# Kernel optimization log

Hardware: AMD Instinct MI355X
Metric: run time of the kernel (lower is better)

Reference implementation:

```python
import jax, jax.numpy as jnp
import numpy as np
from jax import lax

VOCAB = 18
EMB = 200
HID = 200
SEQ = 128
BATCH = 2048
PAD_IDX = 0


def setup_inputs() -> dict:
    key = jax.random.key(0)
    ks = jax.random.split(key, 8)
    s_emb = 1.0  # torch nn.Embedding default N(0,1)
    s_lstm = 1.0 / np.sqrt(HID)  # torch LSTM default U(-1/sqrt(H), 1/sqrt(H))
    s_lin = 1.0 / np.sqrt(HID)
    inp = {
        "x": jax.random.randint(ks[0], (BATCH, SEQ), 0, VOCAB, dtype=jnp.int32),
        "E": jax.random.normal(ks[1], (VOCAB, EMB), dtype=jnp.float32) * s_emb,
        "W_ih": jax.random.uniform(ks[2], (4 * HID, EMB), minval=-s_lstm, maxval=s_lstm, dtype=jnp.float32),
        "W_hh": jax.random.uniform(ks[3], (4 * HID, HID), minval=-s_lstm, maxval=s_lstm, dtype=jnp.float32),
        "b_ih": jax.random.uniform(ks[4], (4 * HID,), minval=-s_lstm, maxval=s_lstm, dtype=jnp.float32),
        "b_hh": jax.random.uniform(ks[5], (4 * HID,), minval=-s_lstm, maxval=s_lstm, dtype=jnp.float32),
        "W_out": jax.random.uniform(ks[6], (VOCAB, HID), minval=-s_lin, maxval=s_lin, dtype=jnp.float32),
        "b_out": jax.random.uniform(ks[7], (VOCAB,), minval=-s_lin, maxval=s_lin, dtype=jnp.float32),
    }
    return inp


def _forward(x, E, W_ih, W_hh, b_ih, b_hh, W_out, b_out):
    # Embedding with padding_idx=0 (row 0 is zero, no grad flows to it)
    pad_mask = (jnp.arange(VOCAB) != PAD_IDX).astype(E.dtype)[:, None]
    emb = (E * pad_mask)[x]  # (B, T, EMB)
    B = emb.shape[0]
    # Precompute input contribution to all gates for every timestep
    x_proj = jnp.einsum("bte,ge->btg", emb, W_ih) + b_ih + b_hh  # (B, T, 4H)

    def step(carry, xg_t):
        h, c = carry
        gates = xg_t + h @ W_hh.T  # (B, 4H)
        i, f, g, o = jnp.split(gates, 4, axis=-1)  # torch gate order i,f,g,o
        i = jax.nn.sigmoid(i)
        f = jax.nn.sigmoid(f)
        g = jnp.tanh(g)
        o = jax.nn.sigmoid(o)
        c = f * c + i * g
        h = o * jnp.tanh(c)
        return (h, c), h

    h0 = jnp.zeros((B, HID), dtype=emb.dtype)
    c0 = jnp.zeros((B, HID), dtype=emb.dtype)
    (h_n, c_n), hs = lax.scan(step, (h0, c0), x_proj.transpose(1, 0, 2))
    out = hs.transpose(1, 0, 2)  # (B, T, HID)
    logits = out @ W_out.T + b_out  # (B, T, VOCAB)
    return logits, h_n, c_n


def reference(x, E, W_ih, W_hh, b_ih, b_hh, W_out, b_out):
    return _forward(x, E, W_ih, W_hh, b_ih, b_hh, W_out, b_out)
```

## Files before the change

### kernel.cpp

```cpp
#include <hip/hip_runtime.h>

#define VOCAB 18
#define EMB   200
#define HID   200
#define G4    800
#define SEQ   128
#define BATCH 2048
#define MB    8
#define NT    56
#define KS    7
#define TPB   256
#define TPW   14
#define SV    (SEQ*VOCAB)
#define LOGITS_N ((size_t)BATCH*SEQ*VOCAB)

typedef short s16x8 __attribute__((ext_vector_type(8)));
typedef short s16x4 __attribute__((ext_vector_type(4)));
typedef float f32x4 __attribute__((ext_vector_type(4)));

__device__ __forceinline__ unsigned short f2bf(float f) {
  unsigned int u = __float_as_uint(f);
  u += 0x7FFFu + ((u >> 16) & 1u);
  return (unsigned short)(u >> 16);
}
__device__ __forceinline__ float sigm(float x) {
  float e = __builtin_amdgcn_exp2f(x * 1.4426950408889634f);
  return e * __builtin_amdgcn_rcpf(e + 1.0f);
}
__device__ __forceinline__ float tanhq(float x) {
  float e = __builtin_amdgcn_exp2f(x * 2.8853900817779268f);
  return 1.0f - 2.0f * __builtin_amdgcn_rcpf(e + 1.0f);
}

__device__ __forceinline__ int oh_elem(int r, int k) {
  return (384 + ((k >> 3) & 3) * 16 + r) * 8 + (k & 7);
}

__global__ void prep_tbl(const float* __restrict__ E, const float* __restrict__ W_ih,
                         const float* __restrict__ b_ih, const float* __restrict__ b_hh,
                         unsigned short* __restrict__ tbl) {
  int tid = blockIdx.x * 256 + threadIdx.x;
  if (tid >= VOCAB * G4) return;
  int v = tid / G4, col = tid % G4;
  float s = b_ih[col] + b_hh[col];
  if (v != 0) {
    const float* Er = E + v * EMB;
    const float* Wr = W_ih + col * EMB;
    for (int e = 0; e < EMB; ++e) s += Er[e] * Wr[e];
  }
  tbl[tid] = f2bf(s);
}

__global__ void prep_wp(const float* __restrict__ W_hh, const float* __restrict__ W_out,
                        const float* __restrict__ b_out,
                        const unsigned short* __restrict__ tbl,
                        short* __restrict__ Wp) {
  int u = blockIdx.x * 256 + threadIdx.x;
  if (u >= NT * KS * 64) return;
  int n    = u / (KS * 64);
  int rem  = u % (KS * 64);
  int s_   = rem >> 6;
  int lane = rem & 63;
  int col  = 16 * n + (lane & 15);
  int kb   = lane >> 4;
  s16x8 o;
  #pragma unroll
  for (int i = 0; i < 8; ++i) {
    int k = 32 * s_ + 8 * kb + i;
    short b = 0;
    if (col < G4) {
      if (k < HID)                          b = (short)f2bf(W_hh[col * HID + k]);
      else if (k >= 201 && k < 201 + VOCAB) b = (short)tbl[(k - 201) * G4 + col];
    } else if (col < G4 + VOCAB) {
      if (k < HID)        b = (short)f2bf(W_out[(col - G4) * HID + k]);
      else if (k == HID)  b = (short)f2bf(b_out[col - G4]);
    }
    o[i] = b;
  }
  *(s16x8*)(Wp + (size_t)u * 8) = o;
}

__global__ __launch_bounds__(TPB) __attribute__((amdgpu_waves_per_eu(1, 1)))
void lstm_kernel(const int* __restrict__ x, const short* __restrict__ Wp,
                 float* __restrict__ out) {
  __shared__ unsigned short hA[KS * 64 * 8];
  __shared__ float gatesL[MB * G4];
  __shared__ int   xtok[MB * SEQ];
  __shared__ float logL[MB * SV];

  const int tid  = threadIdx.x;
  const int lane = tid & 63;
  const int w    = tid >> 6;
  const int blk  = blockIdx.x;
  const int l15  = lane & 15;
  const int rowq = (lane >> 4) << 2;
  const bool lo  = (lane < 32);

  for (int i = tid; i < KS * 64 * 8; i += TPB)
    hA[i] = (i >= 3200 && i < 3264 && (i & 7) == 0) ? (unsigned short)0x3F80
                                                    : (unsigned short)0;
  for (int i = tid; i < MB * SEQ; i += TPB) xtok[i] = x[blk * (MB * SEQ) + i];

  s16x8 wf[TPW][KS];
  #pragma unroll
  for (int n = 0; n < TPW; ++n) {
    #pragma unroll
    for (int s = 0; s < KS; ++s) {
      wf[n][s] = *(const s16x8*)(Wp + ((((w * TPW + n) * KS) + s) * 64 + lane) * 8);
      asm volatile("" : "+a"(wf[n][s]));
    }
    asm volatile("" ::: "memory");
  }

  __syncthreads();
  if (tid < MB) hA[oh_elem(tid, 201 + xtok[tid * SEQ])] = 0x3F80;

  float cA[4] = {0.f, 0.f, 0.f, 0.f};
  float cB[4] = {0.f, 0.f, 0.f, 0.f};
  __syncthreads();

  #pragma unroll 1
  for (int t = 0; t < SEQ; ++t) {
    s16x8 aF[KS];
    #pragma unroll
    for (int s = 0; s < KS; ++s) aF[s] = *(const s16x8*)&hA[(s * 64 + lane) * 8];

    auto store_tile = [&](int n, const f32x4& a) {
      int col = 16 * (w * TPW + n) + l15;
      if (col < G4) {
        #pragma unroll
        for (int q = 0; q < 4; ++q)
          gatesL[(rowq + q) * G4 + col] = a[q];
      } else if (col < G4 + 32 && t > 0) {
        int v = col - G4;
        if (v < VOCAB) {
          #pragma unroll
          for (int q = 0; q < 4; ++q)
            logL[(rowq + q) * SV + (t - 1) * VOCAB + v] = a[q];
        }
      }
    };

    #pragma unroll
    for (int g = 0; g < 2; ++g) {
      f32x4 acc[7];
      #pragma unroll
      for (int j = 0; j < 7; ++j) { acc[j][0]=0.f; acc[j][1]=0.f; acc[j][2]=0.f; acc[j][3]=0.f; }
      #pragma unroll
      for (int s = 0; s < KS; ++s) {
        #pragma unroll
        for (int j = 0; j < 7; ++j)
          acc[j] = __builtin_amdgcn_mfma_f32_16x16x32_bf16(aF[s], wf[g * 7 + j][s], acc[j], 0, 0, 0);
      }
      if (lo) {
        #pragma unroll
        for (int j = 0; j < 7; ++j) store_tile(g * 7 + j, acc[j]);
      }
    }
    __syncthreads();

    auto phaseB = [&](int pk, float (&cc)[4]) {
      int r  = pk / 50;
      int j0 = (pk - r * 50) * 4;
      f32x4 xi = *(const f32x4*)&gatesL[r * G4 + j0];
      f32x4 xf = *(const f32x4*)&gatesL[r * G4 + 200 + j0];
      f32x4 xg = *(const f32x4*)&gatesL[r * G4 + 400 + j0];
      f32x4 xo = *(const f32x4*)&gatesL[r * G4 + 600 + j0];
      s16x4 hp;
      f32x4 hv, cv;
      #pragma unroll
      for (int e = 0; e < 4; ++e) {
        float i_ = sigm(xi[e]);
        float f_ = sigm(xf[e]);
        float g_ = tanhq(xg[e]);
        float o_ = sigm(xo[e]);
        float cn = f_ * cc[e] + i_ * g_;
        float h  = o_ * tanhq(cn);
        cc[e] = cn;
        hp[e] = (short)f2bf(h);
        hv[e] = h; cv[e] = cn;
      }
      int hbase = ((j0 >> 5) * 64 + r + 16 * ((j0 >> 3) & 3)) * 8 + (j0 & 7);
      *(s16x4*)&hA[hbase] = hp;
      if (t == SEQ - 1) {
        size_t bg = (size_t)blk * MB + r;
        *(f32x4*)&out[LOGITS_N + bg * HID + j0] = hv;
        *(f32x4*)&out[LOGITS_N + (size_t)BATCH * HID + bg * HID + j0] = cv;
      }
    };
    phaseB(tid, cA);
    if (tid < 144) phaseB(tid + 256, cB);

    if (tid < MB && t + 1 < SEQ) {
      int v0 = xtok[tid * SEQ + t];
      int v1 = xtok[tid * SEQ + t + 1];
      hA[oh_elem(tid, 201 + v0)] = 0;
      hA[oh_elem(tid, 201 + v1)] = 0x3F80;
    }
    __syncthreads();
  }

  if (w == 3) {
    s16x8 aF[KS];
    #pragma unroll
    for (int s = 0; s < KS; ++s) aF[s] = *(const s16x8*)&hA[(s * 64 + lane) * 8];
    f32x4 a1, a2;
    a1[0]=0.f; a1[1]=0.f; a1[2]=0.f; a1[3]=0.f;
    a2[0]=0.f; a2[1]=0.f; a2[2]=0.f; a2[3]=0.f;
    #pragma unroll
    for (int s = 0; s < KS; ++s) {
      a1 = __builtin_amdgcn_mfma_f32_16x16x32_bf16(aF[s], wf[8][s], a1, 0, 0, 0);
      a2 = __builtin_amdgcn_mfma_f32_16x16x32_bf16(aF[s], wf[9][s], a2, 0, 0, 0);
    }
    if (lo) {
      #pragma unroll
      for (int q = 0; q < 4; ++q) {
        int base = (rowq + q) * SV + (SEQ - 1) * VOCAB;
        if (l15 < VOCAB)      logL[base + l15]      = a1[q];
        if (16 + l15 < VOCAB) logL[base + 16 + l15] = a2[q];
      }
    }
  }
  __syncthreads();

  float* dst = out + (size_t)blk * (MB * SV);
  for (int i = tid * 4; i < MB * SV; i += TPB * 4)
    *(f32x4*)&dst[i] = *(const f32x4*)&logL[i];
}

extern "C" void kernel_launch(void* const* d_in, const int* in_sizes, int n_in,
                              void* d_out, int out_size, void* d_ws, size_t ws_size,
                              hipStream_t stream) {
  const int*   x     = (const int*)  d_in[0];
  const float* E     = (const float*)d_in[1];
  const float* W_ih  = (const float*)d_in[2];
  const float* W_hh  = (const float*)d_in[3];
  const float* b_ih  = (const float*)d_in[4];
  const float* b_hh  = (const float*)d_in[5];
  const float* W_out = (const float*)d_in[6];
  const float* b_out = (const float*)d_in[7];
  float* out = (float*)d_out;

  unsigned short* tbl = (unsigned short*)d_ws;
  short* Wp = (short*)d_ws + VOCAB * G4;

  prep_tbl<<<(VOCAB * G4 + 255) / 256, 256, 0, stream>>>(E, W_ih, b_ih, b_hh, tbl);
  prep_wp<<<(NT * KS * 64 + 255) / 256, 256, 0, stream>>>(W_hh, W_out, b_out, tbl, Wp);
  lstm_kernel<<<BATCH / MB, TPB, 0, stream>>>(x, Wp, out);
}
```

Baseline: 343.5 us.

## Double threads per block to 512, halving weight tiles per wave

Moves the LSTM block from 4 to 8 waves, so each wave holds 7 column tiles of the recurrent weights in registers instead of 14. The gate nonlinearity phase now uses 400 threads, one 4-wide chunk each, instead of 256 threads with a second partial pass. A-fragments are reloaded from shared memory per k-slice rather than kept in registers. This adds MFMA parallelism per CU and shortens each wave's serial step chain, at the cost of more LDS reads and larger barriers.

```diff
diff --git a/kernel.cpp b/kernel.cpp
--- a/kernel.cpp
+++ b/kernel.cpp
@@ -9,8 +9,8 @@
 #define MB    8
 #define NT    56
 #define KS    7
-#define TPB   256
-#define TPW   14
+#define TPB   512
+#define TPW   7
 #define SV    (SEQ*VOCAB)
 #define LOGITS_N ((size_t)BATCH*SEQ*VOCAB)
 
@@ -80,7 +80,7 @@
   *(s16x8*)(Wp + (size_t)u * 8) = o;
 }
 
-__global__ __launch_bounds__(TPB) __attribute__((amdgpu_waves_per_eu(1, 1)))
+__global__ __launch_bounds__(TPB) __attribute__((amdgpu_waves_per_eu(2, 2)))
 void lstm_kernel(const int* __restrict__ x, const short* __restrict__ Wp,
                  float* __restrict__ out) {
   __shared__ unsigned short hA[KS * 64 * 8];
@@ -115,16 +115,11 @@
   __syncthreads();
   if (tid < MB) hA[oh_elem(tid, 201 + xtok[tid * SEQ])] = 0x3F80;
 
-  float cA[4] = {0.f, 0.f, 0.f, 0.f};
-  float cB[4] = {0.f, 0.f, 0.f, 0.f};
+  float creg[4] = {0.f, 0.f, 0.f, 0.f};
   __syncthreads();
 
   #pragma unroll 1
   for (int t = 0; t < SEQ; ++t) {
-    s16x8 aF[KS];
-    #pragma unroll
-    for (int s = 0; s < KS; ++s) aF[s] = *(const s16x8*)&hA[(s * 64 + lane) * 8];
-
     auto store_tile = [&](int n, const f32x4& a) {
       int col = 16 * (w * TPW + n) + l15;
       if (col < G4) {
@@ -141,27 +136,43 @@
       }
     };
 
-    #pragma unroll
-    for (int g = 0; g < 2; ++g) {
-      f32x4 acc[7];
-      #pragma unroll
-      for (int j = 0; j < 7; ++j) { acc[j][0]=0.f; acc[j][1]=0.f; acc[j][2]=0.f; acc[j][3]=0.f; }
+    {
+      f32x4 acc[4];
+      #pragma unroll
+      for (int j = 0; j < 4; ++j) { acc[j][0]=0.f; acc[j][1]=0.f; acc[j][2]=0.f; acc[j][3]=0.f; }
       #pragma unroll
       for (int s = 0; s < KS; ++s) {
-        #pragma unroll
-        for (int j = 0; j < 7; ++j)
-          acc[j] = __builtin_amdgcn_mfma_f32_16x16x32_bf16(aF[s], wf[g * 7 + j][s], acc[j], 0, 0, 0);
+        s16x8 aF = *(const s16x8*)&hA[(s * 64 + lane) * 8];
+        #pragma unroll
+        for (int j = 0; j < 4; ++j)
+          acc[j] = __builtin_amdgcn_mfma_f32_16x16x32_bf16(aF, wf[j][s], acc[j], 0, 0, 0);
       }
       if (lo) {
         #pragma unroll
-        for (int j = 0; j < 7; ++j) store_tile(g * 7 + j, acc[j]);
+        for (int j = 0; j < 4; ++j) store_tile(j, acc[j]);
+      }
+    }
+    {
+      f32x4 acc[3];
+      #pragma unroll
+      for (int j = 0; j < 3; ++j) { acc[j][0]=0.f; acc[j][1]=0.f; acc[j][2]=0.f; acc[j][3]=0.f; }
+      #pragma unroll
+      for (int s = 0; s < KS; ++s) {
+        s16x8 aF = *(const s16x8*)&hA[(s * 64 + lane) * 8];
+        #pragma unroll
+        for (int j = 0; j < 3; ++j)
+          acc[j] = __builtin_amdgcn_mfma_f32_16x16x32_bf16(aF, wf[4 + j][s], acc[j], 0, 0, 0);
+      }
+      if (lo) {
+        #pragma unroll
+        for (int j = 0; j < 3; ++j) store_tile(4 + j, acc[j]);
       }
     }
     __syncthreads();
 
-    auto phaseB = [&](int pk, float (&cc)[4]) {
-      int r  = pk / 50;
-      int j0 = (pk - r * 50) * 4;
+    if (tid < 400) {
+      int r  = tid / 50;
+      int j0 = (tid - r * 50) * 4;
       f32x4 xi = *(const f32x4*)&gatesL[r * G4 + j0];
       f32x4 xf = *(const f32x4*)&gatesL[r * G4 + 200 + j0];
       f32x4 xg = *(const f32x4*)&gatesL[r * G4 + 400 + j0];
@@ -174,9 +185,9 @@
         float f_ = sigm(xf[e]);
         float g_ = tanhq(xg[e]);
         float o_ = sigm(xo[e]);
-        float cn = f_ * cc[e] + i_ * g_;
+        float cn = f_ * creg[e] + i_ * g_;
         float h  = o_ * tanhq(cn);
-        cc[e] = cn;
+        creg[e] = cn;
         hp[e] = (short)f2bf(h);
         hv[e] = h; cv[e] = cn;
       }
@@ -187,10 +198,7 @@
         *(f32x4*)&out[LOGITS_N + bg * HID + j0] = hv;
         *(f32x4*)&out[LOGITS_N + (size_t)BATCH * HID + bg * HID + j0] = cv;
       }
-    };
-    phaseB(tid, cA);
-    if (tid < 144) phaseB(tid + 256, cB);
-
+    }
     if (tid < MB && t + 1 < SEQ) {
       int v0 = xtok[tid * SEQ + t];
       int v1 = xtok[tid * SEQ + t + 1];
@@ -200,7 +208,7 @@
     __syncthreads();
   }
 
-  if (w == 3) {
+  if (w == 7) {
     s16x8 aF[KS];
     #pragma unroll
     for (int s = 0; s < KS; ++s) aF[s] = *(const s16x8*)&hA[(s * 64 + lane) * 8];
@@ -209,8 +217,8 @@
     a2[0]=0.f; a2[1]=0.f; a2[2]=0.f; a2[3]=0.f;
     #pragma unroll
     for (int s = 0; s < KS; ++s) {
-      a1 = __builtin_amdgcn_mfma_f32_16x16x32_bf16(aF[s], wf[8][s], a1, 0, 0, 0);
-      a2 = __builtin_amdgcn_mfma_f32_16x16x32_bf16(aF[s], wf[9][s], a2, 0, 0, 0);
+      a1 = __builtin_amdgcn_mfma_f32_16x16x32_bf16(aF[s], wf[1][s], a1, 0, 0, 0);
+      a2 = __builtin_amdgcn_mfma_f32_16x16x32_bf16(aF[s], wf[2][s], a2, 0, 0, 0);
     }
     if (lo) {
       #pragma unroll
```

After: 342.9 us. No clear change (-0.2%).
